# Performance work log

Hardware: AMD Instinct MI355X
Metric: run time of the kernel (lower is better)

## Reference

```python
import jax, jax.numpy as jnp
import numpy as np

B, T, I, H, C = 128, 1024, 64, 256, 64
OUT_LEN = 128


def setup_inputs() -> dict:
    key = jax.random.key(0)
    ks = jax.random.split(key, 10)
    s_ih = 1.0 / np.sqrt(H)
    inp = {
        "x": jax.random.normal(ks[0], (B, T, I), jnp.float32),
        "lengths": jax.random.randint(ks[1], (B,), 1, T + 1),
        "out_lengths": OUT_LEN,
        # LSTMCell params (PyTorch layout: W [4H, in], gate order i,f,g,o)
        "W_ih": jax.random.uniform(ks[2], (4 * H, I), jnp.float32, -s_ih, s_ih),
        "W_hh": jax.random.uniform(ks[3], (4 * H, H), jnp.float32, -s_ih, s_ih),
        "b_ih": jax.random.uniform(ks[4], (4 * H,), jnp.float32, -s_ih, s_ih),
        "b_hh": jax.random.uniform(ks[5], (4 * H,), jnp.float32, -s_ih, s_ih),
        # fc head: Linear(H,H) -> ReLU -> Linear(H,C)
        "W1": jax.random.uniform(ks[6], (H, H), jnp.float32, -s_ih, s_ih),
        "b1": jax.random.uniform(ks[7], (H,), jnp.float32, -s_ih, s_ih),
        "W2": jax.random.uniform(ks[8], (C, H), jnp.float32, -s_ih, s_ih),
        "b2": jax.random.uniform(ks[9], (C,), jnp.float32, -s_ih, s_ih),
    }
    return inp


def reference(x, lengths, out_lengths, W_ih, W_hh, b_ih, b_hh, W1, b1, W2, b2):
    Bn, Tn, _ = x.shape
    Hn = W_hh.shape[1]
    bias = b_ih + b_hh  # [4H]

    def cell(h, c, gates_x):
        # gates_x already contains x@W_ih^T + biases
        gates = gates_x + h @ W_hh.T  # [B, 4H]
        i, f, g, o = jnp.split(gates, 4, axis=-1)
        c2 = jax.nn.sigmoid(f) * c + jax.nn.sigmoid(i) * jnp.tanh(g)
        h2 = jax.nn.sigmoid(o) * jnp.tanh(c2)
        return h2, c2

    # precompute input projections for all timesteps: [T, B, 4H]
    gates_x = jnp.einsum('bti,gi->tbg', x, W_ih) + bias
    masks = (jnp.arange(Tn)[None, :] < lengths[:, None]).astype(x.dtype).T  # [T, B]

    def enc_step(carry, inp):
        h, c = carry
        gx, m = inp
        h2, c2 = cell(h, c, gx)
        m = m[:, None]
        return (m * h2 + (1.0 - m) * h, m * c2 + (1.0 - m) * c), None

    h0 = jnp.zeros((Bn, Hn), x.dtype)
    c0 = jnp.zeros((Bn, Hn), x.dtype)
    (h, c), _ = jax.lax.scan(enc_step, (h0, c0), (gates_x, masks))

    def dec_step(carry, _):
        h, c = carry
        # decoder input is zeros, so x-projection is just the bias
        h2, c2 = cell(h, c, bias[None, :])
        out = jax.nn.relu(h2 @ W1.T + b1) @ W2.T + b2  # [B, C]
        return (h2, c2), out

    (_, _), outs = jax.lax.scan(dec_step, (h, c), None, length=out_lengths)
    return jnp.transpose(outs, (1, 0, 2))  # [B, out_lengths, C]
```

## Files before the change

### kernel.cpp

```cpp
#include <hip/hip_runtime.h>

#define B_    128
#define T_    1024
#define I_    64
#define H_    256
#define DEC_  128
#define C_    64
#define NWG   128
#define KTOT  320
#define LDK   328
#define STEPS (T_ + DEC_)
#define RING  32
#define SAFE  24

typedef short bf16x8 __attribute__((ext_vector_type(8)));
typedef float f32x4  __attribute__((ext_vector_type(4)));
typedef unsigned u32x4 __attribute__((ext_vector_type(4)));

#define SCOPE_AGENT __HIP_MEMORY_SCOPE_AGENT

__device__ __forceinline__ f32x4 mf(bf16x8 a, bf16x8 b, f32x4 c) {
  return __builtin_amdgcn_mfma_f32_16x16x32_bf16(a, b, c, 0, 0, 0);
}

__device__ __forceinline__ u32x4 load16_coh(const void* p) {
  u32x4 r;
  asm volatile("global_load_dwordx4 %0, %1, off sc0 sc1" : "=v"(r) : "v"(p) : "memory");
  return r;
}
__device__ __forceinline__ void store16_coh(void* p, u32x4 v) {
  asm volatile("global_store_dwordx4 %0, %1, off sc0 sc1" :: "v"(p), "v"(v) : "memory");
}

__device__ __forceinline__ void bf16_split(float v, unsigned short& hi, unsigned short& lo) {
  unsigned u = __float_as_uint(v);
  unsigned r = (u + 0x7fffu + ((u >> 16) & 1u)) & 0xffff0000u;
  hi = (unsigned short)(r >> 16);
  float fl = v - __uint_as_float(r);
  unsigned u2 = __float_as_uint(fl);
  unsigned r2 = (u2 + 0x7fffu + ((u2 >> 16) & 1u)) & 0xffff0000u;
  lo = (unsigned short)(r2 >> 16);
}

__device__ __forceinline__ float sigm(float v) { return 1.0f / (1.0f + __expf(-v)); }
__device__ __forceinline__ float tanh_(float v) {
  float e = __expf(-2.0f * fabsf(v));
  float t = (1.0f - e) / (1.0f + e);
  return (v >= 0.0f) ? t : -t;
}

__global__ __launch_bounds__(256) void xsplit_k(const float* __restrict__ x,
                                                unsigned short* __restrict__ xh,
                                                unsigned short* __restrict__ xl, int n4) {
  const int i = blockIdx.x * 256 + threadIdx.x;
  if (i >= n4) return;
  const float4 v = ((const float4*)x)[i];
  unsigned short h[4], l[4];
  bf16_split(v.x, h[0], l[0]);
  bf16_split(v.y, h[1], l[1]);
  bf16_split(v.z, h[2], l[2]);
  bf16_split(v.w, h[3], l[3]);
  uint2 uh, ul;
  uh.x = (unsigned)h[0] | ((unsigned)h[1] << 16);
  uh.y = (unsigned)h[2] | ((unsigned)h[3] << 16);
  ul.x = (unsigned)l[0] | ((unsigned)l[1] << 16);
  ul.y = (unsigned)l[2] | ((unsigned)l[3] << 16);
  ((uint2*)xh)[i] = uh;
  ((uint2*)xl)[i] = ul;
}

__global__ __launch_bounds__(256, 1) void rnn5(
    const float* __restrict__ x,
    const unsigned short* __restrict__ x_hi,
    const unsigned short* __restrict__ x_lo,
    const int use_xs,
    const int* __restrict__ lengths,
    const float* __restrict__ W_ih, const float* __restrict__ W_hh,
    const float* __restrict__ b_ih, const float* __restrict__ b_hh,
    char* __restrict__ arrb,
    char* __restrict__ ring,
    char* __restrict__ decb)
{
  __shared__ unsigned short Whi[16][LDK];
  __shared__ unsigned short Wlo[16][LDK];

  const int tid  = threadIdx.x;
  const int g    = blockIdx.x;
  const int uo   = g >> 1;
  const int sh   = g & 1;
  const int j0   = uo * 4;
  const int wave = tid >> 6;
  const int lane = tid & 63;
  const int q4   = lane >> 4;
  const int n15  = lane & 15;
  const int s    = sh * 64 + wave * 16 + n15;

  for (int e = tid; e < 16 * KTOT; e += 256) {
    const int row = e / KTOT;
    const int k   = e - row * KTOT;
    const int grow = (row & 3) * H_ + j0 + (row >> 2);
    const float v = (k < H_) ? W_hh[grow * H_ + k] : W_ih[grow * I_ + (k - H_)];
    unsigned short h16, l16; bf16_split(v, h16, l16);
    Whi[row][k] = h16; Wlo[row][k] = l16;
  }
  __syncthreads();

  bf16x8 Ah[10], Al[10];
  #pragma unroll
  for (int kh = 0; kh < 8; ++kh) {
    const int k0 = kh * 32 + q4 * 8;
    Ah[kh] = *(const bf16x8*)&Whi[n15][k0];
    Al[kh] = *(const bf16x8*)&Wlo[n15][k0];
  }
  #pragma unroll
  for (int kx = 0; kx < 2; ++kx) {
    const int k0 = H_ + kx * 32 + q4 * 8;
    Ah[8 + kx] = *(const bf16x8*)&Whi[n15][k0];
    Al[8 + kx] = *(const bf16x8*)&Wlo[n15][k0];
  }
  float bias4[4];
  #pragma unroll
  for (int e = 0; e < 4; ++e) {
    const int grow = e * H_ + j0 + q4;
    bias4[e] = b_ih[grow] + b_hh[grow];
  }

  const int len_s = lengths[s];

  if (tid < 64) {
    const int sz = sh * 64 + tid;
    u32x4 z; z.x = 0u; z.y = 0u; z.z = 0u; z.w = 0u;
    store16_coh(ring + (((size_t)uo * 128 + sz) << 4), z);
  }

  auto xpart = [&](int t, f32x4& a0, f32x4& a1, f32x4& a2) {
    #pragma unroll
    for (int e = 0; e < 4; ++e) { a0[e] = bias4[e]; a1[e] = 0.f; a2[e] = 0.f; }
    if (t >= T_) return;
    #pragma unroll
    for (int kx = 0; kx < 2; ++kx) {
      bf16x8 bh, bl;
      if (use_xs) {
        const int xo = (s * T_ + t) * I_ + kx * 32 + q4 * 8;
        bh = *(const bf16x8*)(x_hi + xo);
        bl = *(const bf16x8*)(x_lo + xo);
      } else {
        const float* xp = x + ((size_t)s * T_ + t) * I_ + kx * 32 + q4 * 8;
        const float4 xa = *(const float4*)xp;
        const float4 xb = *(const float4*)(xp + 4);
        union { bf16x8 v; unsigned short u[8]; } bxh, bxl;
        float xv[8] = {xa.x, xa.y, xa.z, xa.w, xb.x, xb.y, xb.z, xb.w};
        #pragma unroll
        for (int e2 = 0; e2 < 8; ++e2) bf16_split(xv[e2], bxh.u[e2], bxl.u[e2]);
        bh = bxh.v; bl = bxl.v;
      }
      a0 = mf(Ah[8 + kx], bh, a0);
      a1 = mf(Ah[8 + kx], bl, a1);
      a2 = mf(Al[8 + kx], bh, a2);
    }
  };

  f32x4 xa0, xa1, xa2;
  xpart(0, xa0, xa1, xa2);

  float c_st = 0.f;
  float h_st = 0.f;

  for (int t = 0; t < STEPS; ++t) {
    const char* rslot = ring + (size_t)(t & (RING - 1)) * 131072;
    const unsigned eb = (unsigned)((t >> 5) & 1u);

    u32x4 d0,d1,d2,d3,d4,d5,d6,d7,d8,d9,d10,d11,d12,d13,d14,d15;
    for (;;) {
#define LD_KH(i, DA, DB) { \
      const char* _b = rslot + (((size_t)(((i) * 8 + (q4 << 1)) * 128 + s)) << 4); \
      DA = load16_coh(_b); DB = load16_coh(_b + 2048); }
      LD_KH(0, d0,  d1)  LD_KH(1, d2,  d3)  LD_KH(2, d4,  d5)  LD_KH(3, d6,  d7)
      LD_KH(4, d8,  d9)  LD_KH(5, d10, d11) LD_KH(6, d12, d13) LD_KH(7, d14, d15)
#undef LD_KH
      asm volatile("s_waitcnt vmcnt(0)"
        : "+v"(d0),"+v"(d1),"+v"(d2),"+v"(d3),"+v"(d4),"+v"(d5),"+v"(d6),"+v"(d7),
          "+v"(d8),"+v"(d9),"+v"(d10),"+v"(d11),"+v"(d12),"+v"(d13),"+v"(d14),"+v"(d15)
        :: "memory");
      unsigned ok = 1u;
#define CK(D) ok &= (unsigned)((D.z & 1u) == eb);
      CK(d0) CK(d1) CK(d2) CK(d3) CK(d4) CK(d5) CK(d6) CK(d7)
      CK(d8) CK(d9) CK(d10) CK(d11) CK(d12) CK(d13) CK(d14) CK(d15)
#undef CK
      if (__all((int)ok)) break;
    }

    f32x4 a0 = xa0, a1 = xa1, a2 = xa2;
    f32x4 b0, b1, b2;
    #pragma unroll
    for (int e = 0; e < 4; ++e) { b0[e] = 0.f; b1[e] = 0.f; b2[e] = 0.f; }
#define MM_KH(i, ACC0, ACC1, ACC2, DA, DB) { \
    union { u32x4 q; bf16x8 v; } _h, _l; \
    _h.q.x = DA.x; _h.q.y = DA.y; _h.q.z = DB.x; _h.q.w = DB.y; \
    _l.q.x = DA.z; _l.q.y = DA.w; _l.q.z = DB.z; _l.q.w = DB.w; \
    ACC0 = mf(Ah[i], _h.v, ACC0); ACC1 = mf(Ah[i], _l.v, ACC1); ACC2 = mf(Al[i], _h.v, ACC2); }
    MM_KH(0, a0, a1, a2, d0,  d1)  MM_KH(1, a0, a1, a2, d2,  d3)
    MM_KH(2, a0, a1, a2, d4,  d5)  MM_KH(3, a0, a1, a2, d6,  d7)
    MM_KH(4, b0, b1, b2, d8,  d9)  MM_KH(5, b0, b1, b2, d10, d11)
    MM_KH(6, b0, b1, b2, d12, d13) MM_KH(7, b0, b1, b2, d14, d15)
#undef MM_KH

    const bool update = (t < T_) ? (t < len_s) : true;
    const unsigned gnxt = (unsigned)(((t + 1) >> 5) & 15);
    const float gi = (a0[0] + b0[0]) + (a1[0] + b1[0]) + (a2[0] + b2[0]);
    const float gf = (a0[1] + b0[1]) + (a1[1] + b1[1]) + (a2[1] + b2[1]);
    const float gg = (a0[2] + b0[2]) + (a1[2] + b1[2]) + (a2[2] + b2[2]);
    const float go = (a0[3] + b0[3]) + (a1[3] + b1[3]) + (a2[3] + b2[3]);
    const float cn = sigm(gf) * c_st + sigm(gi) * tanh_(gg);
    const float hn = sigm(go) * tanh_(cn);
    c_st = update ? cn : c_st;
    h_st = update ? hn : h_st;

    unsigned short hh, hl;
    bf16_split(h_st, hh, hl);
    hl = (unsigned short)((hl & 0xFFFEu) | ((gnxt >> q4) & 1u));
    const unsigned p  = (unsigned)hh | ((unsigned)hl << 16);
    const unsigned p1 = (unsigned)__shfl_xor((int)p, 16, 64);
    const unsigned p2 = (unsigned)__shfl_xor((int)p, 32, 64);
    const unsigned p3 = (unsigned)__shfl_xor((int)p1, 32, 64);

    u32x4 vh16;
    vh16.x = (p  & 0xFFFFu) | (p1 << 16);
    vh16.y = (p2 & 0xFFFFu) | (p3 << 16);
    vh16.z = (p >> 16)      | (p1 & 0xFFFF0000u);
    vh16.w = (p2 >> 16)     | (p3 & 0xFFFF0000u);
    const size_t chunk_off = ((size_t)uo * 128 + s) << 4;
    if (q4 == 0)
      store16_coh(ring + (size_t)((t + 1) & (RING - 1)) * 131072 + chunk_off, vh16);

    if (t >= T_ && q4 == 0) {
      const int td = t - T_;
      *(u32x4*)(decb + ((((size_t)td * 64 + uo) * 128 + s) << 4)) = vh16;
    }
    xpart(t + 1, xa0, xa1, xa2);

    if ((t % SAFE) == (SAFE - 1)) {
      asm volatile("s_waitcnt vmcnt(0)" ::: "memory");
      const unsigned ep = (unsigned)(t + 1);
      const int wid = g * 4 + wave;
      if (lane == 0)
        __hip_atomic_store((unsigned*)(arrb + (size_t)wid * 128), ep,
                           __ATOMIC_RELAXED, SCOPE_AGENT);
      bool okb;
      do {
        unsigned mn = ~0u;
        #pragma unroll
        for (int j = 0; j < 8; ++j) {
          unsigned v = __hip_atomic_load(
              (const unsigned*)(arrb + (size_t)(lane * 8 + j) * 128),
              __ATOMIC_RELAXED, SCOPE_AGENT);
          mn = (v < mn) ? v : mn;
        }
        okb = (mn >= ep);
      } while (!__all((int)okb));
    }
  }
}

__global__ __launch_bounds__(256) void mlp1(
    const char* __restrict__ decb,
    const float* __restrict__ W1, const float* __restrict__ b1,
    unsigned short* __restrict__ z_hi, unsigned short* __restrict__ z_lo)
{
  __shared__ unsigned short Ahi[32][264];
  __shared__ unsigned short Alo[32][264];
  __shared__ float bias_s[32];
  const int tid  = threadIdx.x;
  const int nblk = blockIdx.x & 7;
  const int mblk = blockIdx.x >> 3;
  const int n0   = nblk * 32;
  const int wave = tid >> 6, lane = tid & 63, q4 = lane >> 4, n15 = lane & 15;

  for (int e = tid; e < 32 * 256; e += 256) {
    const int row = e >> 8, k = e & 255;
    unsigned short h16, l16;
    bf16_split(W1[(n0 + row) * 256 + k], h16, l16);
    Ahi[row][k] = h16; Alo[row][k] = l16;
  }
  if (tid < 32) bias_s[tid] = b1[n0 + tid];
  __syncthreads();

  f32x4 acc[2][2];
  #pragma unroll
  for (int r = 0; r < 2; ++r)
    #pragma unroll
    for (int c = 0; c < 2; ++c)
      #pragma unroll
      for (int e = 0; e < 4; ++e) acc[r][c][e] = bias_s[16 * r + q4 * 4 + e];

  #pragma unroll
  for (int kh = 0; kh < 8; ++kh) {
    const int k0 = kh * 32 + q4 * 8;
    const bf16x8 ah0 = *(const bf16x8*)&Ahi[n15][k0];
    const bf16x8 ah1 = *(const bf16x8*)&Ahi[16 + n15][k0];
    const bf16x8 al0 = *(const bf16x8*)&Alo[n15][k0];
    const bf16x8 al1 = *(const bf16x8*)&Alo[16 + n15][k0];
    const int u0 = (kh * 4 + q4) * 2;
    #pragma unroll
    for (int c = 0; c < 2; ++c) {
      const int sloc = wave * 32 + c * 16 + n15;
      const char* base = decb + ((((size_t)mblk * 64 + u0) * 128 + sloc) << 4);
      const u32x4 A4 = *(const u32x4*)base;
      const u32x4 B4 = *(const u32x4*)(base + 2048);
      union { u32x4 q; bf16x8 v; } bh, bl;
      bh.q.x = A4.x; bh.q.y = A4.y; bh.q.z = B4.x; bh.q.w = B4.y;
      bl.q.x = A4.z; bl.q.y = A4.w; bl.q.z = B4.z; bl.q.w = B4.w;
      acc[0][c] = mf(ah0, bh.v, acc[0][c]);
      acc[1][c] = mf(ah1, bh.v, acc[1][c]);
      acc[0][c] = mf(ah0, bl.v, acc[0][c]);
      acc[1][c] = mf(ah1, bl.v, acc[1][c]);
      acc[0][c] = mf(al0, bh.v, acc[0][c]);
      acc[1][c] = mf(al1, bh.v, acc[1][c]);
    }
  }

  #pragma unroll
  for (int r = 0; r < 2; ++r)
    #pragma unroll
    for (int c = 0; c < 2; ++c) {
      const int sloc = wave * 32 + c * 16 + n15;
      const int m = mblk * 128 + sloc;
      const int ng = n0 + 16 * r + q4 * 4;
      unsigned short hh[4], ll[4];
      #pragma unroll
      for (int e = 0; e < 4; ++e) {
        const float v = fmaxf(acc[r][c][e], 0.0f);
        bf16_split(v, hh[e], ll[e]);
      }
      uint2 uh2, ul2;
      uh2.x = (unsigned)hh[0] | ((unsigned)hh[1] << 16);
      uh2.y = (unsigned)hh[2] | ((unsigned)hh[3] << 16);
      ul2.x = (unsigned)ll[0] | ((unsigned)ll[1] << 16);
      ul2.y = (unsigned)ll[2] | ((unsigned)ll[3] << 16);
      *(uint2*)(z_hi + m * 256 + ng) = uh2;
      *(uint2*)(z_lo + m * 256 + ng) = ul2;
    }
}

__global__ __launch_bounds__(256) void mlp2(
    const unsigned short* __restrict__ z_hi, const unsigned short* __restrict__ z_lo,
    const float* __restrict__ W2, const float* __restrict__ b2,
    float* __restrict__ out)
{
  __shared__ unsigned short Ahi[32][264];
  __shared__ unsigned short Alo[32][264];
  __shared__ float bias_s[32];
  const int tid  = threadIdx.x;
  const int cblk = blockIdx.x & 1;
  const int mblk = blockIdx.x >> 1;
  const int c0   = cblk * 32;
  const int wave = tid >> 6, lane = tid & 63, q4 = lane >> 4, n15 = lane & 15;

  for (int e = tid; e < 32 * 256; e += 256) {
    const int row = e >> 8, k = e & 255;
    unsigned short h16, l16;
    bf16_split(W2[(c0 + row) * 256 + k], h16, l16);
    Ahi[row][k] = h16; Alo[row][k] = l16;
  }
  if (tid < 32) bias_s[tid] = b2[c0 + tid];
  __syncthreads();

  f32x4 acc[2][2];
  #pragma unroll
  for (int r = 0; r < 2; ++r)
    #pragma unroll
    for (int c = 0; c < 2; ++c)
      #pragma unroll
      for (int e = 0; e < 4; ++e) acc[r][c][e] = bias_s[16 * r + q4 * 4 + e];

  #pragma unroll
  for (int kh = 0; kh < 8; ++kh) {
    const int k0 = kh * 32 + q4 * 8;
    const bf16x8 ah0 = *(const bf16x8*)&Ahi[n15][k0];
    const bf16x8 ah1 = *(const bf16x8*)&Ahi[16 + n15][k0];
    const bf16x8 al0 = *(const bf16x8*)&Alo[n15][k0];
    const bf16x8 al1 = *(const bf16x8*)&Alo[16 + n15][k0];
    #pragma unroll
    for (int c = 0; c < 2; ++c) {
      const int m = mblk * 128 + wave * 32 + c * 16 + n15;
      const bf16x8 bh = *(const bf16x8*)(z_hi + m * 256 + k0);
      const bf16x8 bl = *(const bf16x8*)(z_lo + m * 256 + k0);
      acc[0][c] = mf(ah0, bh, acc[0][c]);
      acc[1][c] = mf(ah1, bh, acc[1][c]);
      acc[0][c] = mf(ah0, bl, acc[0][c]);
      acc[1][c] = mf(ah1, bl, acc[1][c]);
      acc[0][c] = mf(al0, bh, acc[0][c]);
      acc[1][c] = mf(al1, bh, acc[1][c]);
    }
  }

  #pragma unroll
  for (int r = 0; r < 2; ++r)
    #pragma unroll
    for (int c = 0; c < 2; ++c) {
      const int m  = mblk * 128 + wave * 32 + c * 16 + n15;
      const int ss = m & 127;
      const int td = m >> 7;
      const int cg = c0 + 16 * r + q4 * 4;
      *(f32x4*)(out + ss * (DEC_ * C_) + td * C_ + cg) = acc[r][c];
    }
}

extern "C" void kernel_launch(void* const* d_in, const int* in_sizes, int n_in,
                              void* d_out, int out_size, void* d_ws, size_t ws_size,
                              hipStream_t stream) {
  (void)in_sizes; (void)n_in; (void)out_size;
  const float* x    = (const float*)d_in[0];
  const int*   lens = (const int*)d_in[1];
  const float* W_ih = (const float*)d_in[3];
  const float* W_hh = (const float*)d_in[4];
  const float* b_ih = (const float*)d_in[5];
  const float* b_hh = (const float*)d_in[6];
  const float* W1   = (const float*)d_in[7];
  const float* b1   = (const float*)d_in[8];
  const float* W2   = (const float*)d_in[9];
  const float* b2   = (const float*)d_in[10];
  float* out = (float*)d_out;

  char* ws8  = (char*)d_ws;
  char* arrb = ws8;
  char* ring = ws8 + 65536;
  char* decb = ws8 + 65536 + (size_t)RING * 131072;

  const size_t decb_end = 65536 + (size_t)RING * 131072 + 16777216ull;
  const size_t NEED_XS  = decb_end + 2ull * 16777216ull;
  const int use_xs = (ws_size >= NEED_XS) ? 1 : 0;

  unsigned short* x_hi; unsigned short* x_lo;
  unsigned short* z_hi; unsigned short* z_lo;
  if (use_xs) {
    x_hi = (unsigned short*)(ws8 + decb_end);
    x_lo = x_hi + (size_t)B_ * T_ * I_;
    z_hi = (unsigned short*)(ws8 + decb_end);
    z_lo = z_hi + (size_t)DEC_ * B_ * H_;
  } else {
    x_hi = nullptr; x_lo = nullptr;
    z_hi = (unsigned short*)(ws8 + decb_end);
    z_lo = z_hi + (size_t)DEC_ * B_ * H_;
  }

  (void)hipMemsetAsync(arrb, 0, 65536, stream);
  (void)hipMemsetAsync(ring, 0xFF, (size_t)RING * 131072, stream);
  if (use_xs) {
    const int n4 = (B_ * T_ * I_) / 4;
    xsplit_k<<<(n4 + 255) / 256, 256, 0, stream>>>(x, x_hi, x_lo, n4);
  }
  rnn5<<<NWG, 256, 0, stream>>>(x, x_hi, x_lo, use_xs, lens,
                                W_ih, W_hh, b_ih, b_hh,
                                arrb, ring, decb);
  mlp1<<<1024, 256, 0, stream>>>(decb, W1, b1, z_hi, z_lo);
  mlp2<<<256, 256, 0, stream>>>(z_hi, z_lo, W2, b2, out);
}
```

Measured before the change: 2.853 ms.

## Sort sequences by length and skip recurrent work for finished waves

Each workgroup ranks the 128 sequences by descending length and maps its wave lanes to those sorted sequences. A wave then skips the ring polling, MFMA gate math and input projection for every encoder step past the longest sequence it owns. It still publishes its frozen hidden state with the epoch bits so the ring protocol stays consistent. Idle waves sleep while polling the periodic barrier, and one shuffle now reads directly from the source lane instead of chaining through another shuffle. The aim is to cut memory and MFMA contention on the latency-bound lockstep loop, but the critical path is still set by the longest sequence.

```diff
diff --git a/kernel.cpp b/kernel.cpp
--- a/kernel.cpp
+++ b/kernel.cpp
@@ -83,6 +83,8 @@
 {
   __shared__ unsigned short Whi[16][LDK];
   __shared__ unsigned short Wlo[16][LDK];
+  __shared__ int len_sh[128];
+  __shared__ int perm_s[128];
 
   const int tid  = threadIdx.x;
   const int g    = blockIdx.x;
@@ -95,6 +97,18 @@
   const int n15  = lane & 15;
   const int s    = sh * 64 + wave * 16 + n15;
 
+  if (tid < 128) len_sh[tid] = lengths[tid];
+  __syncthreads();
+  if (tid < 128) {
+    const int li = len_sh[tid];
+    int rank = 0;
+    for (int j = 0; j < 128; ++j) {
+      const int lj = len_sh[j];
+      rank += (int)((lj > li) || (lj == li && j < tid));
+    }
+    perm_s[rank] = tid;
+  }
+
   for (int e = tid; e < 16 * KTOT; e += 256) {
     const int row = e / KTOT;
     const int k   = e - row * KTOT;
@@ -105,6 +119,10 @@
   }
   __syncthreads();
 
+  const int s_phys = perm_s[s];
+  const int len_s  = len_sh[s_phys];
+  const int gmax   = len_sh[perm_s[sh * 64 + wave * 16]];
+
   bf16x8 Ah[10], Al[10];
   #pragma unroll
   for (int kh = 0; kh < 8; ++kh) {
@@ -125,8 +143,6 @@
     bias4[e] = b_ih[grow] + b_hh[grow];
   }
 
-  const int len_s = lengths[s];
-
   if (tid < 64) {
     const int sz = sh * 64 + tid;
     u32x4 z; z.x = 0u; z.y = 0u; z.z = 0u; z.w = 0u;
@@ -141,11 +157,11 @@
     for (int kx = 0; kx < 2; ++kx) {
       bf16x8 bh, bl;
       if (use_xs) {
-        const int xo = (s * T_ + t) * I_ + kx * 32 + q4 * 8;
+        const int xo = (s_phys * T_ + t) * I_ + kx * 32 + q4 * 8;
         bh = *(const bf16x8*)(x_hi + xo);
         bl = *(const bf16x8*)(x_lo + xo);
       } else {
-        const float* xp = x + ((size_t)s * T_ + t) * I_ + kx * 32 + q4 * 8;
+        const float* xp = x + ((size_t)s_phys * T_ + t) * I_ + kx * 32 + q4 * 8;
         const float4 xa = *(const float4*)xp;
         const float4 xb = *(const float4*)(xp + 4);
         union { bf16x8 v; unsigned short u[8]; } bxh, bxl;
@@ -167,62 +183,67 @@
   float h_st = 0.f;
 
   for (int t = 0; t < STEPS; ++t) {
-    const char* rslot = ring + (size_t)(t & (RING - 1)) * 131072;
-    const unsigned eb = (unsigned)((t >> 5) & 1u);
-
-    u32x4 d0,d1,d2,d3,d4,d5,d6,d7,d8,d9,d10,d11,d12,d13,d14,d15;
-    for (;;) {
+    const bool active = (t < gmax) || (t >= T_);
+
+    if (active) {
+      if (t == T_) xpart(T_, xa0, xa1, xa2);
+      const char* rslot = ring + (size_t)(t & (RING - 1)) * 131072;
+      const unsigned eb = (unsigned)((t >> 5) & 1u);
+
+      u32x4 d0,d1,d2,d3,d4,d5,d6,d7,d8,d9,d10,d11,d12,d13,d14,d15;
+      for (;;) {
 #define LD_KH(i, DA, DB) { \
-      const char* _b = rslot + (((size_t)(((i) * 8 + (q4 << 1)) * 128 + s)) << 4); \
-      DA = load16_coh(_b); DB = load16_coh(_b + 2048); }
-      LD_KH(0, d0,  d1)  LD_KH(1, d2,  d3)  LD_KH(2, d4,  d5)  LD_KH(3, d6,  d7)
-      LD_KH(4, d8,  d9)  LD_KH(5, d10, d11) LD_KH(6, d12, d13) LD_KH(7, d14, d15)
+        const char* _b = rslot + (((size_t)(((i) * 8 + (q4 << 1)) * 128 + s)) << 4); \
+        DA = load16_coh(_b); DB = load16_coh(_b + 2048); }
+        LD_KH(0, d0,  d1)  LD_KH(1, d2,  d3)  LD_KH(2, d4,  d5)  LD_KH(3, d6,  d7)
+        LD_KH(4, d8,  d9)  LD_KH(5, d10, d11) LD_KH(6, d12, d13) LD_KH(7, d14, d15)
 #undef LD_KH
-      asm volatile("s_waitcnt vmcnt(0)"
-        : "+v"(d0),"+v"(d1),"+v"(d2),"+v"(d3),"+v"(d4),"+v"(d5),"+v"(d6),"+v"(d7),
-          "+v"(d8),"+v"(d9),"+v"(d10),"+v"(d11),"+v"(d12),"+v"(d13),"+v"(d14),"+v"(d15)
-        :: "memory");
-      unsigned ok = 1u;
+        asm volatile("s_waitcnt vmcnt(0)"
+          : "+v"(d0),"+v"(d1),"+v"(d2),"+v"(d3),"+v"(d4),"+v"(d5),"+v"(d6),"+v"(d7),
+            "+v"(d8),"+v"(d9),"+v"(d10),"+v"(d11),"+v"(d12),"+v"(d13),"+v"(d14),"+v"(d15)
+          :: "memory");
+        unsigned ok = 1u;
 #define CK(D) ok &= (unsigned)((D.z & 1u) == eb);
-      CK(d0) CK(d1) CK(d2) CK(d3) CK(d4) CK(d5) CK(d6) CK(d7)
-      CK(d8) CK(d9) CK(d10) CK(d11) CK(d12) CK(d13) CK(d14) CK(d15)
+        CK(d0) CK(d1) CK(d2) CK(d3) CK(d4) CK(d5) CK(d6) CK(d7)
+        CK(d8) CK(d9) CK(d10) CK(d11) CK(d12) CK(d13) CK(d14) CK(d15)
 #undef CK
-      if (__all((int)ok)) break;
-    }
-
-    f32x4 a0 = xa0, a1 = xa1, a2 = xa2;
-    f32x4 b0, b1, b2;
-    #pragma unroll
-    for (int e = 0; e < 4; ++e) { b0[e] = 0.f; b1[e] = 0.f; b2[e] = 0.f; }
+        if (__all((int)ok)) break;
+      }
+
+      f32x4 a0 = xa0, a1 = xa1, a2 = xa2;
+      f32x4 b0, b1, b2;
+      #pragma unroll
+      for (int e = 0; e < 4; ++e) { b0[e] = 0.f; b1[e] = 0.f; b2[e] = 0.f; }
 #define MM_KH(i, ACC0, ACC1, ACC2, DA, DB) { \
-    union { u32x4 q; bf16x8 v; } _h, _l; \
-    _h.q.x = DA.x; _h.q.y = DA.y; _h.q.z = DB.x; _h.q.w = DB.y; \
-    _l.q.x = DA.z; _l.q.y = DA.w; _l.q.z = DB.z; _l.q.w = DB.w; \
-    ACC0 = mf(Ah[i], _h.v, ACC0); ACC1 = mf(Ah[i], _l.v, ACC1); ACC2 = mf(Al[i], _h.v, ACC2); }
-    MM_KH(0, a0, a1, a2, d0,  d1)  MM_KH(1, a0, a1, a2, d2,  d3)
-    MM_KH(2, a0, a1, a2, d4,  d5)  MM_KH(3, a0, a1, a2, d6,  d7)
-    MM_KH(4, b0, b1, b2, d8,  d9)  MM_KH(5, b0, b1, b2, d10, d11)
-    MM_KH(6, b0, b1, b2, d12, d13) MM_KH(7, b0, b1, b2, d14, d15)
+      union { u32x4 q; bf16x8 v; } _h, _l; \
+      _h.q.x = DA.x; _h.q.y = DA.y; _h.q.z = DB.x; _h.q.w = DB.y; \
+      _l.q.x = DA.z; _l.q.y = DA.w; _l.q.z = DB.z; _l.q.w = DB.w; \
+      ACC0 = mf(Ah[i], _h.v, ACC0); ACC1 = mf(Ah[i], _l.v, ACC1); ACC2 = mf(Al[i], _h.v, ACC2); }
+      MM_KH(0, a0, a1, a2, d0,  d1)  MM_KH(1, a0, a1, a2, d2,  d3)
+      MM_KH(2, a0, a1, a2, d4,  d5)  MM_KH(3, a0, a1, a2, d6,  d7)
+      MM_KH(4, b0, b1, b2, d8,  d9)  MM_KH(5, b0, b1, b2, d10, d11)
+      MM_KH(6, b0, b1, b2, d12, d13) MM_KH(7, b0, b1, b2, d14, d15)
 #undef MM_KH
 
-    const bool update = (t < T_) ? (t < len_s) : true;
+      const bool update = (t < T_) ? (t < len_s) : true;
+      const float gi = (a0[0] + b0[0]) + (a1[0] + b1[0]) + (a2[0] + b2[0]);
+      const float gf = (a0[1] + b0[1]) + (a1[1] + b1[1]) + (a2[1] + b2[1]);
+      const float gg = (a0[2] + b0[2]) + (a1[2] + b1[2]) + (a2[2] + b2[2]);
+      const float go = (a0[3] + b0[3]) + (a1[3] + b1[3]) + (a2[3] + b2[3]);
+      const float cn = sigm(gf) * c_st + sigm(gi) * tanh_(gg);
+      const float hn = sigm(go) * tanh_(cn);
+      c_st = update ? cn : c_st;
+      h_st = update ? hn : h_st;
+    }
+
     const unsigned gnxt = (unsigned)(((t + 1) >> 5) & 15);
-    const float gi = (a0[0] + b0[0]) + (a1[0] + b1[0]) + (a2[0] + b2[0]);
-    const float gf = (a0[1] + b0[1]) + (a1[1] + b1[1]) + (a2[1] + b2[1]);
-    const float gg = (a0[2] + b0[2]) + (a1[2] + b1[2]) + (a2[2] + b2[2]);
-    const float go = (a0[3] + b0[3]) + (a1[3] + b1[3]) + (a2[3] + b2[3]);
-    const float cn = sigm(gf) * c_st + sigm(gi) * tanh_(gg);
-    const float hn = sigm(go) * tanh_(cn);
-    c_st = update ? cn : c_st;
-    h_st = update ? hn : h_st;
-
     unsigned short hh, hl;
     bf16_split(h_st, hh, hl);
     hl = (unsigned short)((hl & 0xFFFEu) | ((gnxt >> q4) & 1u));
     const unsigned p  = (unsigned)hh | ((unsigned)hl << 16);
     const unsigned p1 = (unsigned)__shfl_xor((int)p, 16, 64);
     const unsigned p2 = (unsigned)__shfl_xor((int)p, 32, 64);
-    const unsigned p3 = (unsigned)__shfl_xor((int)p1, 32, 64);
+    const unsigned p3 = (unsigned)__shfl_xor((int)p, 48, 64);
 
     u32x4 vh16;
     vh16.x = (p  & 0xFFFFu) | (p1 << 16);
@@ -233,11 +254,13 @@
     if (q4 == 0)
       store16_coh(ring + (size_t)((t + 1) & (RING - 1)) * 131072 + chunk_off, vh16);
 
-    if (t >= T_ && q4 == 0) {
-      const int td = t - T_;
-      *(u32x4*)(decb + ((((size_t)td * 64 + uo) * 128 + s) << 4)) = vh16;
-    }
-    xpart(t + 1, xa0, xa1, xa2);
+    if (active) {
+      if (t >= T_ && q4 == 0) {
+        const int td = t - T_;
+        *(u32x4*)(decb + ((((size_t)td * 64 + uo) * 128 + s_phys) << 4)) = vh16;
+      }
+      xpart(t + 1, xa0, xa1, xa2);
+    }
 
     if ((t % SAFE) == (SAFE - 1)) {
       asm volatile("s_waitcnt vmcnt(0)" ::: "memory");
@@ -256,8 +279,9 @@
               __ATOMIC_RELAXED, SCOPE_AGENT);
           mn = (v < mn) ? v : mn;
         }
-        okb = (mn >= ep);
-      } while (!__all((int)okb));
+        okb = __all((int)(mn >= ep));
+        if (!okb && !active) __builtin_amdgcn_s_sleep(32);
+      } while (!okb);
     }
   }
 }
```

Measured after the change: 3.047 ms. +6.8%, slower.
